# Performance work log

Hardware: AMD Instinct MI355X
Metric: run time of the kernel (lower is better)

Reference implementation:

```python
import jax, jax.numpy as jnp
import numpy as np

BATCH = 4096
DIM = 256
TEMPERATURE = 0.5
EPS = 1e-8  # torch CosineSimilarity norm clamp


def setup_inputs() -> dict:
    key = jax.random.key(0)
    k1, k2 = jax.random.split(key)
    zA = jax.random.normal(k1, (BATCH, DIM), dtype=jnp.float32)
    zB = jax.random.normal(k2, (BATCH, DIM), dtype=jnp.float32)
    return {"zA": zA, "zB": zB}


def reference(zA, zB):
    b = zA.shape[0]
    N = 2 * b
    z = jnp.concatenate([zA, zB], axis=0)                      # [N, D]
    norm = jnp.maximum(jnp.linalg.norm(z, axis=1, keepdims=True), EPS)
    zn = z / norm
    # cosine-similarity matrix via normalize + GEMM (same math as the
    # broadcasted CosineSimilarity(dim=2) in the original)
    sim = (zn @ zn.T) / TEMPERATURE                            # [N, N]

    idx = jnp.arange(N)
    pos = sim[idx, (idx + b) % N]                              # diag(+b) ++ diag(-b)

    # CE with label 0 over logits=[pos, negatives]; the logit set per row is
    # exactly {all j != i} (pos partner included once), so mask only the diagonal.
    neg_inf = jnp.finfo(sim.dtype).min
    masked = jnp.where(jnp.eye(N, dtype=bool), neg_inf, sim)
    per_row = jax.nn.logsumexp(masked, axis=1) - pos           # [N]
    loss = jnp.sum(per_row) / N                                # reduction='sum' / N
    return loss
```

## Files before the change

### kernel.cpp

```cpp
#include <hip/hip_runtime.h>
#include <hip/hip_bf16.h>

#define N_ROWS 8192
#define BATCH 4096
#define DIM 256

#define NB 64
#define BR 128
#define CT 16
#define NT 8
#define NBLK (NB * (NB + 1) / 2)
#define LDSROW 528
#define LDSBUF (CT * LDSROW)
#define KEXP 2.8853900817779268f

typedef __attribute__((ext_vector_type(8))) short bfrag8;
typedef __attribute__((ext_vector_type(4))) float facc4;

__global__ __launch_bounds__(256) void normalize_kernel(
    const float* __restrict__ zA, const float* __restrict__ zB,
    __hip_bfloat16* __restrict__ zn) {
    int tid = threadIdx.x;
    int wave = tid >> 6, lane = tid & 63;
    int row = blockIdx.x * 4 + wave;
    const float* src = (row < BATCH) ? (zA + (size_t)row * DIM)
                                     : (zB + (size_t)(row - BATCH) * DIM);
    float4 v = ((const float4*)src)[lane];
    float ss = v.x * v.x + v.y * v.y + v.z * v.z + v.w * v.w;
    #pragma unroll
    for (int m = 32; m; m >>= 1) ss += __shfl_xor(ss, m);
    float inv = 1.0f / fmaxf(sqrtf(ss), 1e-8f);
    union { ushort4 u; __hip_bfloat16 h[4]; } o;
    o.h[0] = __float2bfloat16(v.x * inv);
    o.h[1] = __float2bfloat16(v.y * inv);
    o.h[2] = __float2bfloat16(v.z * inv);
    o.h[3] = __float2bfloat16(v.w * inv);
    ((ushort4*)zn)[(size_t)row * (DIM / 4) + lane] = o.u;
}

__global__ __launch_bounds__(256, 3) void ntxent_main(
    const __hip_bfloat16* __restrict__ zn_,
    float* __restrict__ ep, float* __restrict__ pp) {
    const char* zn = (const char*)zn_;
    __shared__ char lds[2 * LDSBUF] __attribute__((aligned(16)));
    __shared__ float colbuf[4][BR];
    int tid = threadIdx.x, lane = tid & 63, wave = tid >> 6;
    int quad = lane >> 4, l15 = lane & 15;

    int bid = blockIdx.x;
    int k = (bid & 7) * (NBLK / 8) + (bid >> 3);

    int bi = (int)(0.5f * (129.0f - sqrtf(16641.0f - 8.0f * (float)k)));
    if (bi < 0) bi = 0;
    if (bi > NB - 1) bi = NB - 1;
    while (bi * (129 - bi) / 2 > k) --bi;
    while ((bi + 1) * (128 - bi) / 2 <= k) ++bi;
    int bj = bi + (k - bi * (129 - bi) / 2);
    bool diagblk = (bi == bj);

    int row0 = bi * BR + wave * 32;

    int col0 = tid >> 5, j0 = tid & 31;
    unsigned lofs0 = col0 * LDSROW + j0 * 16;
    unsigned lofs1 = (col0 + 8) * LDSROW + j0 * 16;
    unsigned gofs0 = col0 * 512 + j0 * 16;
    unsigned gofs1 = (col0 + 8) * 512 + j0 * 16;
    const char* gbase = zn + (size_t)bj * BR * 512;

    uint4 p0 = *(const uint4*)(gbase + gofs0);
    uint4 p1 = *(const uint4*)(gbase + gofs1);

    bfrag8 a[2][8];
    #pragma unroll
    for (int s = 0; s < 2; s++) {
        const char* ap = zn + (size_t)(row0 + s * 16 + l15) * 512 + quad * 16;
        #pragma unroll
        for (int ks = 0; ks < 8; ks++)
            a[s][ks] = *(const bfrag8*)(ap + ks * 64);
    }

    float es[2][4];
    #pragma unroll
    for (int s = 0; s < 2; s++)
        #pragma unroll
        for (int r = 0; r < 4; r++) es[s][r] = 0.f;

    *(uint4*)(lds + lofs0) = p0;
    *(uint4*)(lds + lofs1) = p1;
    __syncthreads();

    for (int t = 0; t < NT; t++) {
        char* cur = lds + (t & 1) * LDSBUF;
        char* nxt = lds + ((t + 1) & 1) * LDSBUF;
        uint4 s0, s1;
        if (t + 1 < NT) {
            const char* g = gbase + (size_t)(t + 1) * CT * 512;
            s0 = *(const uint4*)(g + gofs0);
            s1 = *(const uint4*)(g + gofs1);
        }
        const char* bp = cur + l15 * LDSROW + quad * 16;
        bfrag8 bf[8];
        #pragma unroll
        for (int ks = 0; ks < 8; ks++)
            bf[ks] = *(const bfrag8*)(bp + ks * 64);

        facc4 acc[2];
        acc[0] = (facc4){0.f, 0.f, 0.f, 0.f};
        acc[1] = (facc4){0.f, 0.f, 0.f, 0.f};
        #pragma unroll
        for (int ks = 0; ks < 8; ks++) {
            acc[0] = __builtin_amdgcn_mfma_f32_16x16x32_bf16(a[0][ks], bf[ks], acc[0], 0, 0, 0);
            acc[1] = __builtin_amdgcn_mfma_f32_16x16x32_bf16(a[1][ks], bf[ks], acc[1], 0, 0, 0);
        }

        int ctile = bj * BR + t * CT;
        int gcol = ctile + l15;
        float ce = 0.0f;
        bool isdiag = (ctile >> 5) == (row0 >> 5);
        bool ispos  = (ctile >> 5) == ((row0 ^ BATCH) >> 5);

        if (isdiag) {
            #pragma unroll
            for (int s = 0; s < 2; s++)
                #pragma unroll
                for (int r = 0; r < 4; r++) {
                    int grow = row0 + s * 16 + quad * 4 + r;
                    float e = __builtin_amdgcn_exp2f(acc[s][r] * KEXP);
                    if (gcol == grow) e = 0.0f;
                    es[s][r] += e; ce += e;
                }
        } else {
            #pragma unroll
            for (int s = 0; s < 2; s++)
                #pragma unroll
                for (int r = 0; r < 4; r++) {
                    float e = __builtin_amdgcn_exp2f(acc[s][r] * KEXP);
                    es[s][r] += e; ce += e;
                }
            if (ispos) {
                #pragma unroll
                for (int s = 0; s < 2; s++)
                    #pragma unroll
                    for (int r = 0; r < 4; r++) {
                        int grow = row0 + s * 16 + quad * 4 + r;
                        if (gcol == (grow ^ BATCH)) {
                            float d = acc[s][r];
                            pp[grow] = d;
                            pp[grow ^ BATCH] = d;
                        }
                    }
            }
        }

        if (!diagblk) {
            ce += __shfl_xor(ce, 16);
            ce += __shfl_xor(ce, 32);
            if (lane < 16) colbuf[wave][t * CT + l15] = ce;
        }

        if (t + 1 < NT) {
            *(uint4*)(nxt + lofs0) = s0;
            *(uint4*)(nxt + lofs1) = s1;
        }
        __syncthreads();
    }

    #pragma unroll
    for (int s = 0; s < 2; s++)
        #pragma unroll
        for (int r = 0; r < 4; r++) {
            float e = es[s][r];
            #pragma unroll
            for (int m = 1; m < 16; m <<= 1) e += __shfl_xor(e, m);
            if (l15 == 0)
                ep[(size_t)bj * N_ROWS + row0 + s * 16 + quad * 4 + r] = e;
        }

    if (!diagblk && tid < BR) {
        float v = colbuf[0][tid] + colbuf[1][tid] + colbuf[2][tid] + colbuf[3][tid];
        ep[(size_t)bi * N_ROWS + bj * BR + tid] = v;
    }
}

__global__ __launch_bounds__(256) void finalize_kernel(
    const float* __restrict__ ep, const float* __restrict__ pp,
    float* __restrict__ out) {
    int tid = threadIdx.x;
    int i = blockIdx.x * 256 + tid;
    float e = 0.0f;
    #pragma unroll
    for (int s = 0; s < NB; s++) e += ep[(size_t)s * N_ROWS + i];
    float v = __logf(e) - 2.0f * pp[i];
    #pragma unroll
    for (int m = 32; m; m >>= 1) v += __shfl_xor(v, m);
    __shared__ float wsum[4];
    if ((tid & 63) == 0) wsum[tid >> 6] = v;
    __syncthreads();
    if (tid == 0)
        atomicAdd(out, (wsum[0] + wsum[1] + wsum[2] + wsum[3]) * (1.0f / N_ROWS));
}

extern "C" void kernel_launch(void* const* d_in, const int* in_sizes, int n_in,
                              void* d_out, int out_size, void* d_ws, size_t ws_size,
                              hipStream_t stream) {
    const float* zA = (const float*)d_in[0];
    const float* zB = (const float*)d_in[1];
    float* out = (float*)d_out;
    char* ws = (char*)d_ws;
    __hip_bfloat16* zn = (__hip_bfloat16*)ws;
    float* ep = (float*)(ws + (size_t)N_ROWS * DIM * 2);
    float* pp = ep + (size_t)NB * N_ROWS;

    hipMemsetAsync(out, 0, sizeof(float), stream);
    normalize_kernel<<<N_ROWS / 4, 256, 0, stream>>>(zA, zB, zn);
    ntxent_main<<<NBLK, 256, 0, stream>>>(zn, ep, pp);
    finalize_kernel<<<N_ROWS / 256, 256, 0, stream>>>(ep, pp, out);
}
```

Measured before the change: 119.4 us.

## Load B fragments directly from global into registers, drop LDS staging

Replaces the LDS double-buffered staging of column tiles with per-wave direct global loads of B fragments into two register buffers, ping-ponged across an unrolled tile loop. This removes the LDS writes, LDS reads and per-tile block barriers, adding a single barrier before the column-sum reduction. The cost is that each of the four waves now loads the same B tile from global/L2 separately, which quadruples L2 traffic for B, and the extra fragment registers raise register pressure.

After: 168.7 us. 1.41x slower.

```diff
diff --git a/kernel.cpp b/kernel.cpp
--- a/kernel.cpp
+++ b/kernel.cpp
@@ -10,8 +10,6 @@
 #define CT 16
 #define NT 8
 #define NBLK (NB * (NB + 1) / 2)
-#define LDSROW 528
-#define LDSBUF (CT * LDSROW)
 #define KEXP 2.8853900817779268f
 
 typedef __attribute__((ext_vector_type(8))) short bfrag8;
@@ -42,7 +40,6 @@
     const __hip_bfloat16* __restrict__ zn_,
     float* __restrict__ ep, float* __restrict__ pp) {
     const char* zn = (const char*)zn_;
-    __shared__ char lds[2 * LDSBUF] __attribute__((aligned(16)));
     __shared__ float colbuf[4][BR];
     int tid = threadIdx.x, lane = tid & 63, wave = tid >> 6;
     int quad = lane >> 4, l15 = lane & 15;
@@ -60,15 +57,12 @@
 
     int row0 = bi * BR + wave * 32;
 
-    int col0 = tid >> 5, j0 = tid & 31;
-    unsigned lofs0 = col0 * LDSROW + j0 * 16;
-    unsigned lofs1 = (col0 + 8) * LDSROW + j0 * 16;
-    unsigned gofs0 = col0 * 512 + j0 * 16;
-    unsigned gofs1 = (col0 + 8) * 512 + j0 * 16;
-    const char* gbase = zn + (size_t)bj * BR * 512;
-
-    uint4 p0 = *(const uint4*)(gbase + gofs0);
-    uint4 p1 = *(const uint4*)(gbase + gofs1);
+    const char* gB = zn + (size_t)(bj * BR + l15) * 512 + quad * 16;
+
+    bfrag8 bfA[8], bfB[8];
+    #pragma unroll
+    for (int ks = 0; ks < 8; ks++)
+        bfA[ks] = *(const bfrag8*)(gB + ks * 64);
 
     bfrag8 a[2][8];
     #pragma unroll
@@ -85,25 +79,7 @@
         #pragma unroll
         for (int r = 0; r < 4; r++) es[s][r] = 0.f;
 
-    *(uint4*)(lds + lofs0) = p0;
-    *(uint4*)(lds + lofs1) = p1;
-    __syncthreads();
-
-    for (int t = 0; t < NT; t++) {
-        char* cur = lds + (t & 1) * LDSBUF;
-        char* nxt = lds + ((t + 1) & 1) * LDSBUF;
-        uint4 s0, s1;
-        if (t + 1 < NT) {
-            const char* g = gbase + (size_t)(t + 1) * CT * 512;
-            s0 = *(const uint4*)(g + gofs0);
-            s1 = *(const uint4*)(g + gofs1);
-        }
-        const char* bp = cur + l15 * LDSROW + quad * 16;
-        bfrag8 bf[8];
-        #pragma unroll
-        for (int ks = 0; ks < 8; ks++)
-            bf[ks] = *(const bfrag8*)(bp + ks * 64);
-
+    auto compute_tile = [&](int t, bfrag8 (&bf)[8]) {
         facc4 acc[2];
         acc[0] = (facc4){0.f, 0.f, 0.f, 0.f};
         acc[1] = (facc4){0.f, 0.f, 0.f, 0.f};
@@ -112,7 +88,6 @@
             acc[0] = __builtin_amdgcn_mfma_f32_16x16x32_bf16(a[0][ks], bf[ks], acc[0], 0, 0, 0);
             acc[1] = __builtin_amdgcn_mfma_f32_16x16x32_bf16(a[1][ks], bf[ks], acc[1], 0, 0, 0);
         }
-
         int ctile = bj * BR + t * CT;
         int gcol = ctile + l15;
         float ce = 0.0f;
@@ -151,18 +126,27 @@
                     }
             }
         }
-
         if (!diagblk) {
             ce += __shfl_xor(ce, 16);
             ce += __shfl_xor(ce, 32);
             if (lane < 16) colbuf[wave][t * CT + l15] = ce;
         }
-
-        if (t + 1 < NT) {
-            *(uint4*)(nxt + lofs0) = s0;
-            *(uint4*)(nxt + lofs1) = s1;
-        }
-        __syncthreads();
+    };
+
+    #pragma unroll
+    for (int t = 0; t < NT; t += 2) {
+        const char* g1 = gB + (size_t)(t + 1) * CT * 512;
+        #pragma unroll
+        for (int ks = 0; ks < 8; ks++)
+            bfB[ks] = *(const bfrag8*)(g1 + ks * 64);
+        compute_tile(t, bfA);
+        if (t + 2 < NT) {
+            const char* g2 = gB + (size_t)(t + 2) * CT * 512;
+            #pragma unroll
+            for (int ks = 0; ks < 8; ks++)
+                bfA[ks] = *(const bfrag8*)(g2 + ks * 64);
+        }
+        compute_tile(t + 1, bfB);
     }
 
     #pragma unroll
@@ -176,6 +160,7 @@
                 ep[(size_t)bj * N_ROWS + row0 + s * 16 + quad * 4 + r] = e;
         }
 
+    __syncthreads();
     if (!diagblk && tid < BR) {
         float v = colbuf[0][tid] + colbuf[1][tid] + colbuf[2][tid] + colbuf[3][tid];
         ep[(size_t)bi * N_ROWS + bj * BR + tid] = v;
```
